# Kernel optimization log

Hardware: AMD Instinct MI355X
Metric: run time of the kernel (lower is better)

The kernel has to match this reference:

```python
import jax, jax.numpy as jnp
import numpy as np

B, N, D, K = 1024, 8192, 256, 8
LAMBDA_MULT = 0.01

def setup_inputs() -> dict:
    key = jax.random.key(0)
    k1, k2, k3, k4, k5 = jax.random.split(key, 5)
    x = jax.random.uniform(k1, (B, D), dtype=jnp.float32)
    mu = jax.random.uniform(k2, (N, D), dtype=jnp.float32)
    lambda_base = jax.random.uniform(k3, (N,), dtype=jnp.float32) * LAMBDA_MULT
    v = jax.random.normal(k4, (N, K, D), dtype=jnp.float32)  # stands in for per-unit orthogonal init
    omega = 0.1 + 0.4 * jax.random.uniform(k5, (N, K), dtype=jnp.float32)
    return {"x": x, "mu": mu, "lambda_base": lambda_base, "v": v, "omega": omega}

def reference(x, mu, lambda_base, v, omega):
    # quad_form = diff^T (lambda*I + sum_k omega_k v_k v_k^T) diff
    #           = lambda * ||x - mu||^2 + sum_k omega_k * ((x - mu) . v_k)^2
    # Woodbury-style expansion avoids materializing W:(n,d,d) and diff:(b,n,d).
    x2 = jnp.sum(x * x, axis=-1)                      # (b,)
    mu2 = jnp.sum(mu * mu, axis=-1)                   # (n,)
    xm = x @ mu.T                                     # (b,n)
    sqdist = x2[:, None] - 2.0 * xm + mu2[None, :]    # (b,n) = ||x-mu||^2
    xv = jnp.einsum('bd,nkd->bnk', x, v)              # (b,n,k)
    muv = jnp.einsum('nd,nkd->nk', mu, v)             # (n,k)
    proj2 = (xv - muv[None, :, :]) ** 2               # (b,n,k)
    quad = lambda_base[None, :] * sqdist + jnp.einsum('bnk,nk->bn', proj2, omega)
    return jnp.exp(-quad / D)  # Type == 'exp'
```

## Files before the change

kernel.cpp:

```cpp
#include <hip/hip_runtime.h>


#define B_SZ 1024
#define N_SZ 8192
#define D_SZ 256
#define K_SZ 8

#define BT 128
#define NT 16

typedef __bf16 bf16x8 __attribute__((ext_vector_type(8)));
typedef float f32x4 __attribute__((ext_vector_type(4)));
typedef unsigned short u16x4 __attribute__((ext_vector_type(4)));
typedef unsigned short u16x8 __attribute__((ext_vector_type(8)));

#define WS_X2   0u
#define WS_MU2  4096u
#define WS_MUV  36864u
#define WS_PX   299008u
#define WS_PW   823296u
#define WS_NEED (823296ull + 37748736ull)

__device__ __forceinline__ float wave_reduce(float s) {
#pragma unroll
  for (int off = 32; off > 0; off >>= 1) s += __shfl_down(s, off);
  return s;
}

__device__ __forceinline__ u16x4 cvt4(float4 t) {
  u16x4 r;
  r[0] = __builtin_bit_cast(unsigned short, (__bf16)t.x);
  r[1] = __builtin_bit_cast(unsigned short, (__bf16)t.y);
  r[2] = __builtin_bit_cast(unsigned short, (__bf16)t.z);
  r[3] = __builtin_bit_cast(unsigned short, (__bf16)t.w);
  return r;
}

__device__ __forceinline__ void glds16(const void* g, const void* l) {
  __builtin_amdgcn_global_load_lds(
      (const __attribute__((address_space(1))) void*)g,
      (__attribute__((address_space(3))) void*)l, 16, 0, 0);
}

__global__ void prep_x(const float* __restrict__ x, float* __restrict__ x2,
                       unsigned short* __restrict__ px) {
  const int w = threadIdx.x >> 6, lane = threadIdx.x & 63;
  const int b = blockIdx.x * 4 + w;
  float4 t = *(const float4*)(x + (size_t)b * D_SZ + 4 * lane);
  *(u16x4*)(px + (size_t)b * D_SZ + 4 * lane) = cvt4(t);
  float s = t.x * t.x + t.y * t.y + t.z * t.z + t.w * t.w;
  s = wave_reduce(s);
  if (lane == 0) x2[b] = s;
}

__global__ void prep_w(const float* __restrict__ mu, const float* __restrict__ v,
                       float* __restrict__ mu2, float* __restrict__ muv,
                       unsigned short* __restrict__ pw) {
  __shared__ __align__(16) float mulds[D_SZ];
  const int n = blockIdx.x;
  const int w = threadIdx.x >> 6, lane = threadIdx.x & 63;
  if (w == 0) {
    float4 m4 = *(const float4*)(mu + (size_t)n * D_SZ + 4 * lane);
    *(float4*)(mulds + 4 * lane) = m4;
    *(u16x4*)(pw + (size_t)n * 9 * D_SZ + 4 * lane) = cvt4(m4);
    float s = m4.x * m4.x + m4.y * m4.y + m4.z * m4.z + m4.w * m4.w;
    s = wave_reduce(s);
    if (lane == 0) mu2[n] = s;
  }
  __syncthreads();
  float4 m4 = *(const float4*)(mulds + 4 * lane);
#pragma unroll
  for (int kk = 0; kk < 2; ++kk) {
    const int k = w * 2 + kk;
    float4 v4 = *(const float4*)(v + ((size_t)n * K_SZ + k) * D_SZ + 4 * lane);
    *(u16x4*)(pw + ((size_t)n * 9 + k + 1) * D_SZ + 4 * lane) = cvt4(v4);
    float s = m4.x * v4.x + m4.y * v4.y + m4.z * v4.z + m4.w * v4.w;
    s = wave_reduce(s);
    if (lane == 0) muv[n * K_SZ + k] = s;
  }
}

__global__ __launch_bounds__(256, 2)
void hmu_main_p(const unsigned short* __restrict__ px,
                const unsigned short* __restrict__ pw,
                const float* __restrict__ lam, const float* __restrict__ om,
                const float* __restrict__ wsf, float* __restrict__ out) {
  __shared__ __align__(16) unsigned short As[BT * 32];
  __shared__ __align__(16) unsigned short Bs[NT * 9 * 32];

  const float* ws_x2 = wsf;
  const float* ws_mu2 = wsf + 1024;
  const float* ws_muv = wsf + 9216;

  const int tid = threadIdx.x;
  const int lane = tid & 63;
  const int w = tid >> 6;
  const int m = lane & 15;
  const int kg = lane >> 4;
  const int nl4 = lane >> 2;
  const int ch = lane & 3;

  const int n0 = blockIdx.x * NT;
  const int b0 = blockIdx.y * BT;

  f32x4 acc[2][9];
#pragma unroll
  for (int bs = 0; bs < 2; ++bs)
#pragma unroll
    for (int j = 0; j < 9; ++j) acc[bs][j] = (f32x4){0.f, 0.f, 0.f, 0.f};

  for (int kt = 0; kt < 8; ++kt) {
    const int k0 = kt * 32;
#pragma unroll
    for (int t = 0; t < 2; ++t) {
      int r0 = w * 32 + t * 16;
      glds16(px + (size_t)(b0 + r0 + nl4) * D_SZ + k0 + ch * 8, As + r0 * 32);
    }
#pragma unroll
    for (int t = 0; t < 3; ++t) {
      int i = w + 4 * t;
      if (i < 9)
        glds16(pw + ((size_t)(n0 + nl4) * 9 + i) * D_SZ + k0 + ch * 8,
               Bs + i * 16 * 32);
    }
    __syncthreads();

    bf16x8 af[2];
#pragma unroll
    for (int bs = 0; bs < 2; ++bs)
      af[bs] = *(const bf16x8*)&As[((2 * w + bs) * 16 + m) * 32 + kg * 8];
#pragma unroll
    for (int j = 0; j < 9; ++j) {
      bf16x8 bfr = *(const bf16x8*)&Bs[(j * 16 + m) * 32 + kg * 8];
      acc[0][j] = __builtin_amdgcn_mfma_f32_16x16x32_bf16(af[0], bfr, acc[0][j], 0, 0, 0);
      acc[1][j] = __builtin_amdgcn_mfma_f32_16x16x32_bf16(af[1], bfr, acc[1][j], 0, 0, 0);
    }
    __syncthreads();
  }

  const int n = n0 + m;
  const float lam_n = lam[n];
  const float mu2_n = ws_mu2[n];
  float omr[8], muvr[8];
#pragma unroll
  for (int k = 0; k < 8; ++k) {
    omr[k] = om[n * 8 + k];
    muvr[k] = ws_muv[n * 8 + k];
  }
#pragma unroll
  for (int bs = 0; bs < 2; ++bs) {
#pragma unroll
    for (int r = 0; r < 4; ++r) {
      int b = b0 + (2 * w + bs) * 16 + kg * 4 + r;
      float x2b = ws_x2[b];
      float c0 = acc[bs][0][r];
      float q = lam_n * (x2b - 2.f * c0 + mu2_n);
#pragma unroll
      for (int k = 0; k < 8; ++k) {
        float p = acc[bs][k + 1][r] - muvr[k];
        q = fmaf(omr[k] * p, p, q);
      }
      out[(size_t)b * N_SZ + n] = __expf(q * (-1.0f / 256.0f));
    }
  }
}

__device__ __forceinline__ void cvt16_store(const float* __restrict__ src,
                                            unsigned short* dst) {
  const float4* p4 = (const float4*)src;
  float fv[16];
#pragma unroll
  for (int e = 0; e < 4; ++e) {
    float4 t = p4[e];
    fv[4 * e + 0] = t.x; fv[4 * e + 1] = t.y;
    fv[4 * e + 2] = t.z; fv[4 * e + 3] = t.w;
  }
  u16x8 lo, hi;
#pragma unroll
  for (int e = 0; e < 8; ++e) {
    lo[e] = __builtin_bit_cast(unsigned short, (__bf16)fv[e]);
    hi[e] = __builtin_bit_cast(unsigned short, (__bf16)fv[e + 8]);
  }
  *(u16x8*)dst = lo;
  *(u16x8*)(dst + 8) = hi;
}

#define LDS_STRIDE 40
__global__ __launch_bounds__(256, 2)
void hmu_main_f(const float* __restrict__ x, const float* __restrict__ mu,
                const float* __restrict__ lam, const float* __restrict__ v,
                const float* __restrict__ om, const float* __restrict__ ws,
                float* __restrict__ out) {
  __shared__ __align__(16) unsigned short As[BT * LDS_STRIDE];
  __shared__ __align__(16) unsigned short Bs[NT * 9 * LDS_STRIDE];
  const float* ws_x2 = ws;
  const float* ws_mu2 = ws + 1024;
  const float* ws_muv = ws + 9216;
  const int tid = threadIdx.x, lane = tid & 63, w = tid >> 6;
  const int m = lane & 15, kg = lane >> 4;
  const int n0 = blockIdx.x * NT, b0 = blockIdx.y * BT;
  f32x4 acc[2][9];
#pragma unroll
  for (int bs = 0; bs < 2; ++bs)
#pragma unroll
    for (int j = 0; j < 9; ++j) acc[bs][j] = (f32x4){0.f, 0.f, 0.f, 0.f};
  const int arow = tid >> 1, ahalf = tid & 1;
  for (int kt = 0; kt < 8; ++kt) {
    const int k0 = kt * 32;
    cvt16_store(x + (size_t)(b0 + arow) * D_SZ + k0 + ahalf * 16,
                &As[arow * LDS_STRIDE + ahalf * 16]);
#pragma unroll
    for (int it = 0; it < 2; ++it) {
      int idx = tid + 256 * it;
      if (idx < 288) {
        int row = idx >> 1, half = idx & 1;
        int nl = row / 9, j = row - nl * 9;
        const float* src = (j == 0)
            ? mu + (size_t)(n0 + nl) * D_SZ + k0 + half * 16
            : v + (size_t)((n0 + nl) * K_SZ + (j - 1)) * D_SZ + k0 + half * 16;
        cvt16_store(src, &Bs[row * LDS_STRIDE + half * 16]);
      }
    }
    __syncthreads();
    bf16x8 af[2];
#pragma unroll
    for (int bs = 0; bs < 2; ++bs)
      af[bs] = *(const bf16x8*)&As[((2 * w + bs) * 16 + m) * LDS_STRIDE + kg * 8];
#pragma unroll
    for (int j = 0; j < 9; ++j) {
      bf16x8 bfr = *(const bf16x8*)&Bs[(m * 9 + j) * LDS_STRIDE + kg * 8];
      acc[0][j] = __builtin_amdgcn_mfma_f32_16x16x32_bf16(af[0], bfr, acc[0][j], 0, 0, 0);
      acc[1][j] = __builtin_amdgcn_mfma_f32_16x16x32_bf16(af[1], bfr, acc[1][j], 0, 0, 0);
    }
    __syncthreads();
  }
  const int n = n0 + m;
  const float lam_n = lam[n];
  const float mu2_n = ws_mu2[n];
  float omr[8], muvr[8];
#pragma unroll
  for (int k = 0; k < 8; ++k) {
    omr[k] = om[n * 8 + k];
    muvr[k] = ws_muv[n * 8 + k];
  }
#pragma unroll
  for (int bs = 0; bs < 2; ++bs)
#pragma unroll
    for (int r = 0; r < 4; ++r) {
      int b = b0 + (2 * w + bs) * 16 + kg * 4 + r;
      float c0 = acc[bs][0][r];
      float q = lam_n * (ws_x2[b] - 2.f * c0 + mu2_n);
#pragma unroll
      for (int k = 0; k < 8; ++k) {
        float p = acc[bs][k + 1][r] - muvr[k];
        q = fmaf(omr[k] * p, p, q);
      }
      out[(size_t)b * N_SZ + n] = __expf(q * (-1.0f / 256.0f));
    }
}

__global__ void p2_mu_f(const float* __restrict__ mu, const float* __restrict__ v,
                        float* __restrict__ mu2, float* __restrict__ muv) {
  __shared__ __align__(16) float mulds[D_SZ];
  const int n = blockIdx.x;
  const int w = threadIdx.x >> 6, lane = threadIdx.x & 63;
  if (w == 0) {
    float4 m4 = *(const float4*)(mu + (size_t)n * D_SZ + 4 * lane);
    *(float4*)(mulds + 4 * lane) = m4;
    float s = m4.x * m4.x + m4.y * m4.y + m4.z * m4.z + m4.w * m4.w;
    s = wave_reduce(s);
    if (lane == 0) mu2[n] = s;
  }
  __syncthreads();
  float4 m4 = *(const float4*)(mulds + 4 * lane);
#pragma unroll
  for (int kk = 0; kk < 2; ++kk) {
    const int k = w * 2 + kk;
    float4 v4 = *(const float4*)(v + ((size_t)n * K_SZ + k) * D_SZ + 4 * lane);
    float s = m4.x * v4.x + m4.y * v4.y + m4.z * v4.z + m4.w * v4.w;
    s = wave_reduce(s);
    if (lane == 0) muv[n * K_SZ + k] = s;
  }
}

__global__ void p1_x2_f(const float* __restrict__ x, float* __restrict__ x2) {
  const int w = threadIdx.x >> 6, lane = threadIdx.x & 63;
  const int b = blockIdx.x * 4 + w;
  float4 t = *(const float4*)(x + (size_t)b * D_SZ + 4 * lane);
  float s = t.x * t.x + t.y * t.y + t.z * t.z + t.w * t.w;
  s = wave_reduce(s);
  if (lane == 0) x2[b] = s;
}

extern "C" void kernel_launch(void* const* d_in, const int* in_sizes, int n_in,
                              void* d_out, int out_size, void* d_ws, size_t ws_size,
                              hipStream_t stream) {
  const float* x   = (const float*)d_in[0];
  const float* mu  = (const float*)d_in[1];
  const float* lam = (const float*)d_in[2];
  const float* v   = (const float*)d_in[3];
  const float* om  = (const float*)d_in[4];
  float* out = (float*)d_out;
  char* wsb = (char*)d_ws;
  float* wsf = (float*)d_ws;
  float* x2  = (float*)(wsb + WS_X2);
  float* mu2 = (float*)(wsb + WS_MU2);
  float* muv = (float*)(wsb + WS_MUV);

  dim3 grid(N_SZ / NT, B_SZ / BT);
  if (ws_size >= WS_NEED) {
    unsigned short* px = (unsigned short*)(wsb + WS_PX);
    unsigned short* pw = (unsigned short*)(wsb + WS_PW);
    prep_x<<<B_SZ / 4, 256, 0, stream>>>(x, x2, px);
    prep_w<<<N_SZ, 256, 0, stream>>>(mu, v, mu2, muv, pw);
    hmu_main_p<<<grid, 256, 0, stream>>>(px, pw, lam, om, wsf, out);
  } else {
    p1_x2_f<<<B_SZ / 4, 256, 0, stream>>>(x, x2);
    p2_mu_f<<<N_SZ, 256, 0, stream>>>(mu, v, mu2, muv);
    hmu_main_f<<<grid, 256, 0, stream>>>(x, mu, lam, v, om, wsf, out);
  }
}
```

Before: 170.9 us.

## Merge prep kernels, double-buffer LDS tiles with XOR swizzle, raise occupancy

The two preprocessing kernels become one launch: each wave handles either one x row or one full mu/v unit, with no LDS or block sync. The main GEMM kernel double-buffers its A/B LDS tiles so the next k-slice's global_load_lds is issued before the current slice's MFMAs, removing one barrier per iteration. It also XOR-swizzles the 16-byte chunk index within rows to cut LDS bank conflicts, and launch bounds rise from 2 to 4 blocks per CU. Doubling LDS and the tighter register budget could cause spills or limit the occupancy actually reached.

```diff
diff --git a/kernel.cpp b/kernel.cpp
--- a/kernel.cpp
+++ b/kernel.cpp
@@ -42,51 +42,69 @@
       (__attribute__((address_space(3))) void*)l, 16, 0, 0);
 }
 
-__global__ void prep_x(const float* __restrict__ x, float* __restrict__ x2,
-                       unsigned short* __restrict__ px) {
+__global__ void prep_all(const float* __restrict__ x, const float* __restrict__ mu,
+                         const float* __restrict__ v,
+                         float* __restrict__ x2, unsigned short* __restrict__ px,
+                         float* __restrict__ mu2, float* __restrict__ muv,
+                         unsigned short* __restrict__ pw) {
   const int w = threadIdx.x >> 6, lane = threadIdx.x & 63;
-  const int b = blockIdx.x * 4 + w;
-  float4 t = *(const float4*)(x + (size_t)b * D_SZ + 4 * lane);
-  *(u16x4*)(px + (size_t)b * D_SZ + 4 * lane) = cvt4(t);
-  float s = t.x * t.x + t.y * t.y + t.z * t.z + t.w * t.w;
-  s = wave_reduce(s);
-  if (lane == 0) x2[b] = s;
-}
-
-__global__ void prep_w(const float* __restrict__ mu, const float* __restrict__ v,
-                       float* __restrict__ mu2, float* __restrict__ muv,
-                       unsigned short* __restrict__ pw) {
-  __shared__ __align__(16) float mulds[D_SZ];
-  const int n = blockIdx.x;
-  const int w = threadIdx.x >> 6, lane = threadIdx.x & 63;
-  if (w == 0) {
+  const int g = blockIdx.x * 4 + w;
+  if (g < B_SZ) {
+    const int b = g;
+    float4 t = *(const float4*)(x + (size_t)b * D_SZ + 4 * lane);
+    *(u16x4*)(px + (size_t)b * D_SZ + 4 * lane) = cvt4(t);
+    float s = t.x * t.x + t.y * t.y + t.z * t.z + t.w * t.w;
+    s = wave_reduce(s);
+    if (lane == 0) x2[b] = s;
+  } else {
+    const int n = g - B_SZ;
     float4 m4 = *(const float4*)(mu + (size_t)n * D_SZ + 4 * lane);
-    *(float4*)(mulds + 4 * lane) = m4;
     *(u16x4*)(pw + (size_t)n * 9 * D_SZ + 4 * lane) = cvt4(m4);
-    float s = m4.x * m4.x + m4.y * m4.y + m4.z * m4.z + m4.w * m4.w;
-    s = wave_reduce(s);
-    if (lane == 0) mu2[n] = s;
-  }
-  __syncthreads();
-  float4 m4 = *(const float4*)(mulds + 4 * lane);
-#pragma unroll
-  for (int kk = 0; kk < 2; ++kk) {
-    const int k = w * 2 + kk;
-    float4 v4 = *(const float4*)(v + ((size_t)n * K_SZ + k) * D_SZ + 4 * lane);
-    *(u16x4*)(pw + ((size_t)n * 9 + k + 1) * D_SZ + 4 * lane) = cvt4(v4);
-    float s = m4.x * v4.x + m4.y * v4.y + m4.z * v4.z + m4.w * v4.w;
-    s = wave_reduce(s);
-    if (lane == 0) muv[n * K_SZ + k] = s;
-  }
-}
-
-__global__ __launch_bounds__(256, 2)
+    float s2 = m4.x * m4.x + m4.y * m4.y + m4.z * m4.z + m4.w * m4.w;
+    float dk[K_SZ];
+#pragma unroll
+    for (int k = 0; k < K_SZ; ++k) {
+      float4 v4 = *(const float4*)(v + ((size_t)n * K_SZ + k) * D_SZ + 4 * lane);
+      *(u16x4*)(pw + ((size_t)n * 9 + k + 1) * D_SZ + 4 * lane) = cvt4(v4);
+      dk[k] = m4.x * v4.x + m4.y * v4.y + m4.z * v4.z + m4.w * v4.w;
+    }
+    s2 = wave_reduce(s2);
+    if (lane == 0) mu2[n] = s2;
+#pragma unroll
+    for (int k = 0; k < K_SZ; ++k) {
+      float r = wave_reduce(dk[k]);
+      if (lane == 0) muv[n * K_SZ + k] = r;
+    }
+  }
+}
+
+__device__ __forceinline__ void stage_tile(const unsigned short* __restrict__ px,
+                                           const unsigned short* __restrict__ pw,
+                                           unsigned short* As, unsigned short* Bs,
+                                           int b0, int n0, int k0, int w, int lane) {
+  const int nl4 = lane >> 2;
+  const int ch = lane & 3;
+  const int kc = (ch ^ ((nl4 >> 1) & 3)) * 8;
+#pragma unroll
+  for (int t = 0; t < 2; ++t) {
+    int r0 = w * 32 + t * 16;
+    glds16(px + (size_t)(b0 + r0 + nl4) * D_SZ + k0 + kc, As + r0 * 32);
+  }
+#pragma unroll
+  for (int t = 0; t < 3; ++t) {
+    int i = w + 4 * t;
+    if (i < 9)
+      glds16(pw + ((size_t)(n0 + nl4) * 9 + i) * D_SZ + k0 + kc, Bs + i * 16 * 32);
+  }
+}
+
+__global__ __launch_bounds__(256, 4)
 void hmu_main_p(const unsigned short* __restrict__ px,
                 const unsigned short* __restrict__ pw,
                 const float* __restrict__ lam, const float* __restrict__ om,
                 const float* __restrict__ wsf, float* __restrict__ out) {
-  __shared__ __align__(16) unsigned short As[BT * 32];
-  __shared__ __align__(16) unsigned short Bs[NT * 9 * 32];
+  __shared__ __align__(16) unsigned short As[2][BT * 32];
+  __shared__ __align__(16) unsigned short Bs[2][NT * 9 * 32];
 
   const float* ws_x2 = wsf;
   const float* ws_mu2 = wsf + 1024;
@@ -97,8 +115,6 @@
   const int w = tid >> 6;
   const int m = lane & 15;
   const int kg = lane >> 4;
-  const int nl4 = lane >> 2;
-  const int ch = lane & 3;
 
   const int n0 = blockIdx.x * NT;
   const int b0 = blockIdx.y * BT;
@@ -109,33 +125,27 @@
 #pragma unroll
     for (int j = 0; j < 9; ++j) acc[bs][j] = (f32x4){0.f, 0.f, 0.f, 0.f};
 
+  const int sw = (kg ^ ((m >> 1) & 3)) * 8;
+
+  stage_tile(px, pw, As[0], Bs[0], b0, n0, 0, w, lane);
+  __syncthreads();
+
   for (int kt = 0; kt < 8; ++kt) {
-    const int k0 = kt * 32;
-#pragma unroll
-    for (int t = 0; t < 2; ++t) {
-      int r0 = w * 32 + t * 16;
-      glds16(px + (size_t)(b0 + r0 + nl4) * D_SZ + k0 + ch * 8, As + r0 * 32);
-    }
-#pragma unroll
-    for (int t = 0; t < 3; ++t) {
-      int i = w + 4 * t;
-      if (i < 9)
-        glds16(pw + ((size_t)(n0 + nl4) * 9 + i) * D_SZ + k0 + ch * 8,
-               Bs + i * 16 * 32);
-    }
-    __syncthreads();
-
-    bf16x8 af[2];
-#pragma unroll
-    for (int bs = 0; bs < 2; ++bs)
-      af[bs] = *(const bf16x8*)&As[((2 * w + bs) * 16 + m) * 32 + kg * 8];
+    const int cur = kt & 1;
+    if (kt < 7)
+      stage_tile(px, pw, As[cur ^ 1], Bs[cur ^ 1], b0, n0, (kt + 1) * 32, w, lane);
+
+    const unsigned short* Ac = As[cur];
+    const unsigned short* Bc = Bs[cur];
+    bf16x8 af0 = *(const bf16x8*)&Ac[((2 * w + 0) * 16 + m) * 32 + sw];
+    bf16x8 af1 = *(const bf16x8*)&Ac[((2 * w + 1) * 16 + m) * 32 + sw];
 #pragma unroll
     for (int j = 0; j < 9; ++j) {
-      bf16x8 bfr = *(const bf16x8*)&Bs[(j * 16 + m) * 32 + kg * 8];
-      acc[0][j] = __builtin_amdgcn_mfma_f32_16x16x32_bf16(af[0], bfr, acc[0][j], 0, 0, 0);
-      acc[1][j] = __builtin_amdgcn_mfma_f32_16x16x32_bf16(af[1], bfr, acc[1][j], 0, 0, 0);
-    }
-    __syncthreads();
+      bf16x8 bfr = *(const bf16x8*)&Bc[(j * 16 + m) * 32 + sw];
+      acc[0][j] = __builtin_amdgcn_mfma_f32_16x16x32_bf16(af0, bfr, acc[0][j], 0, 0, 0);
+      acc[1][j] = __builtin_amdgcn_mfma_f32_16x16x32_bf16(af1, bfr, acc[1][j], 0, 0, 0);
+    }
+    if (kt < 7) __syncthreads();
   }
 
   const int n = n0 + m;
@@ -311,8 +321,7 @@
   if (ws_size >= WS_NEED) {
     unsigned short* px = (unsigned short*)(wsb + WS_PX);
     unsigned short* pw = (unsigned short*)(wsb + WS_PW);
-    prep_x<<<B_SZ / 4, 256, 0, stream>>>(x, x2, px);
-    prep_w<<<N_SZ, 256, 0, stream>>>(mu, v, mu2, muv, pw);
+    prep_all<<<(B_SZ + N_SZ) / 4, 256, 0, stream>>>(x, mu, v, x2, px, mu2, muv, pw);
     hmu_main_p<<<grid, 256, 0, stream>>>(px, pw, lam, om, wsf, out);
   } else {
     p1_x2_f<<<B_SZ / 4, 256, 0, stream>>>(x, x2);
```

New measurement: 209.6 us. +22.7%, slower.
